# Performance work log

Hardware: AMD Instinct MI355X
Metric: run time of the kernel (lower is better)

Reference implementation:

```python
import jax, jax.numpy as jnp
import numpy as np

EPS = 1e-6

def rms_norm(x, scale):
    # T5-style LayerNorm: RMS over last axis in fp32, then scale
    x32 = x.astype(jnp.float32)
    mean2 = jnp.mean(jnp.square(x32), axis=-1, keepdims=True)
    return (x32 * jax.lax.rsqrt(mean2 + EPS)) * scale

def setup_inputs() -> dict:
    key = jax.random.key(0)
    ks = jax.random.split(key, 7)
    B, S, E, H, D = 2, 2048, 2048, 16, 128
    w_std = 1.0 / np.sqrt(E)
    x = jax.random.normal(ks[0], (B, S, E), jnp.float32)
    wq = jax.random.normal(ks[1], (E, H, D), jnp.float32) * w_std
    wk = jax.random.normal(ks[2], (E, H, D), jnp.float32) * w_std
    wv = jax.random.normal(ks[3], (E, H, D), jnp.float32) * w_std
    wo = jax.random.normal(ks[4], (H, D, E), jnp.float32) * (1.0 / np.sqrt(H * D))
    q_scale = jnp.ones((D,), jnp.float32)
    k_scale = jnp.ones((D,), jnp.float32)
    return {"x": x, "wq": wq, "wk": wk, "wv": wv, "wo": wo,
            "q_scale": q_scale, "k_scale": k_scale}

def reference(x, wq, wk, wv, wo, q_scale, k_scale):
    # Q/K/V projections: [B,S,E] x [E,H,D] -> [B,S,H,D]
    q = jnp.einsum('bse,ehd->bshd', x, wq)
    k = jnp.einsum('bse,ehd->bshd', x, wk)
    v = jnp.einsum('bse,ehd->bshd', x, wv)
    # QK layernorm (RMS, no scaling by 1/sqrt(d) in this variant)
    qn = rms_norm(q, q_scale)
    kn = rms_norm(k, k_scale)
    # Naive attention: explicit [B,H,Q,K] scores
    scores = jnp.einsum('bqhd,bkhd->bhqk', qn, kn)
    attn = jax.nn.softmax(scores, axis=-1)
    out = jnp.einsum('bhqk,bkhd->bqhd', attn, v)
    # Output projection: [B,S,H,D] x [H,D,E] -> [B,S,E]
    return jnp.einsum('bqhd,hde->bqe', out, wo)
```

## Files before the change

### kernel.cpp

```cpp
#include <hip/hip_runtime.h>
#include <hip/hip_bf16.h>
#include <math.h>

#define BATCH 2
#define SEQ   2048
#define EMB   2048
#define NH    16
#define HD    128

typedef __attribute__((ext_vector_type(8))) short short8;
typedef __attribute__((ext_vector_type(8))) _Float16 half8;
typedef __attribute__((ext_vector_type(4))) float floatx4;

__device__ inline void async_load16(const void* g, void* l) {
    __builtin_amdgcn_global_load_lds(
        (const __attribute__((address_space(1))) unsigned int*)g,
        (__attribute__((address_space(3))) unsigned int*)l, 16, 0, 0);
}

__device__ inline unsigned short bf16_bits(float f) {
    __hip_bfloat16 b = __float2bfloat16(f);
    return *(unsigned short*)&b;
}
__device__ inline unsigned short fp16_bits(float f) {
    _Float16 h = (_Float16)f;
    return *(unsigned short*)&h;
}

#define GT 128
#define GK 32

__global__ __launch_bounds__(256) void gemm_bf16(
    const unsigned short* __restrict__ A,
    const unsigned short* __restrict__ Bt,
    float* __restrict__ C, int M, int N, int K)
{
    __shared__ unsigned short As[GT * GK];
    __shared__ unsigned short Bs[GT * GK];

    const int tid  = threadIdx.x;
    const int w    = tid >> 6;
    const int lane = tid & 63;
    const int wr   = w >> 1, wc = w & 1;
    const int row0 = blockIdx.y * GT;
    const int col0 = blockIdx.x * GT;

    floatx4 acc[4][4];
    #pragma unroll
    for (int i = 0; i < 4; i++)
        #pragma unroll
        for (int j = 0; j < 4; j++)
            acc[i][j] = (floatx4){0.f, 0.f, 0.f, 0.f};

    const int srow  = lane >> 2;
    const int skoff = (lane & 3) * 8;
    const int fm = lane & 15;
    const int fk = (lane >> 4) * 8;

    for (int k0 = 0; k0 < K; k0 += GK) {
        #pragma unroll
        for (int t = 0; t < 2; t++) {
            const int c = w * 2 + t;
            async_load16(A  + (size_t)(row0 + c * 16 + srow) * K + k0 + skoff, (char*)As + c * 1024);
            async_load16(Bt + (size_t)(col0 + c * 16 + srow) * K + k0 + skoff, (char*)Bs + c * 1024);
        }
        __syncthreads();

        short8 af[4], bf[4];
        #pragma unroll
        for (int i = 0; i < 4; i++) {
            af[i] = *(const short8*)&As[(wr * 64 + i * 16 + fm) * GK + fk];
            bf[i] = *(const short8*)&Bs[(wc * 64 + i * 16 + fm) * GK + fk];
        }
        #pragma unroll
        for (int i = 0; i < 4; i++)
            #pragma unroll
            for (int j = 0; j < 4; j++)
                acc[i][j] = __builtin_amdgcn_mfma_f32_16x16x32_bf16(af[i], bf[j], acc[i][j], 0, 0, 0);
        __syncthreads();
    }

    const int quad = lane >> 4;
    #pragma unroll
    for (int i = 0; i < 4; i++)
        #pragma unroll
        for (int j = 0; j < 4; j++) {
            const size_t base = (size_t)(row0 + wr * 64 + i * 16 + quad * 4) * N
                              + col0 + wc * 64 + j * 16 + fm;
            #pragma unroll
            for (int r = 0; r < 4; r++)
                C[base + (size_t)r * N] = acc[i][j][r];
        }
}

__global__ __launch_bounds__(256) void gemm_qkv(
    const unsigned short* __restrict__ A,
    const unsigned short* __restrict__ Bq, const unsigned short* __restrict__ Bk,
    const unsigned short* __restrict__ Bv,
    const float* __restrict__ q_scale, const float* __restrict__ k_scale,
    unsigned short* __restrict__ Qf, unsigned short* __restrict__ Kf,
    unsigned short* __restrict__ Vt, int K)
{
    __shared__ char smem[2 * 128 * 72 * 2] __attribute__((aligned(16)));
    unsigned short* As = (unsigned short*)smem;
    unsigned short* Bs = (unsigned short*)(smem + 8192);
    float* ws2f = (float*)(smem + 16384);
    typedef unsigned short stage_row[72];
    stage_row* stage0 = (stage_row*)smem;

    const int z = blockIdx.z;
    const unsigned short* __restrict__ Bt = (z == 0) ? Bq : (z == 1) ? Bk : Bv;

    const int tid  = threadIdx.x;
    const int w    = tid >> 6;
    const int lane = tid & 63;
    const int wr   = w >> 1, wc = w & 1;
    const int row0 = blockIdx.y * GT;
    const int col0 = blockIdx.x * GT;

    floatx4 acc[4][4];
    #pragma unroll
    for (int i = 0; i < 4; i++)
        #pragma unroll
        for (int j = 0; j < 4; j++)
            acc[i][j] = (floatx4){0.f, 0.f, 0.f, 0.f};

    const int srow  = lane >> 2;
    const int skoff = (lane & 3) * 8;
    const int fm = lane & 15;
    const int fk = (lane >> 4) * 8;

    for (int k0 = 0; k0 < K; k0 += GK) {
        #pragma unroll
        for (int t = 0; t < 2; t++) {
            const int c = w * 2 + t;
            async_load16(A  + (size_t)(row0 + c * 16 + srow) * K + k0 + skoff, (char*)As + c * 1024);
            async_load16(Bt + (size_t)(col0 + c * 16 + srow) * K + k0 + skoff, (char*)Bs + c * 1024);
        }
        __syncthreads();

        half8 af[4], bf[4];
        #pragma unroll
        for (int i = 0; i < 4; i++) {
            af[i] = *(const half8*)&As[(wr * 64 + i * 16 + fm) * GK + fk];
            bf[i] = *(const half8*)&Bs[(wc * 64 + i * 16 + fm) * GK + fk];
        }
        #pragma unroll
        for (int i = 0; i < 4; i++)
            #pragma unroll
            for (int j = 0; j < 4; j++)
                acc[i][j] = __builtin_amdgcn_mfma_f32_16x16x32_f16(af[i], bf[j], acc[i][j], 0, 0, 0);
        __syncthreads();
    }

    const int quad = lane >> 4;
    const int hh = col0 >> 7;

    if (z < 2) {
        const float* __restrict__ scale = z ? k_scale : q_scale;
        unsigned short* __restrict__ o = z ? Kf : Qf;

        float sq[4][4];
        #pragma unroll
        for (int i = 0; i < 4; i++)
            #pragma unroll
            for (int r = 0; r < 4; r++) {
                float s2 = 0.f;
                #pragma unroll
                for (int j = 0; j < 4; j++) s2 += acc[i][j][r] * acc[i][j][r];
                s2 += __shfl_xor(s2, 1);
                s2 += __shfl_xor(s2, 2);
                s2 += __shfl_xor(s2, 4);
                s2 += __shfl_xor(s2, 8);
                sq[i][r] = s2;
            }
        if (fm == 0) {
            #pragma unroll
            for (int i = 0; i < 4; i++)
                #pragma unroll
                for (int r = 0; r < 4; r++)
                    ws2f[wc * 128 + wr * 64 + i * 16 + quad * 4 + r] = sq[i][r];
        }
        __syncthreads();

        float scv[4];
        #pragma unroll
        for (int j = 0; j < 4; j++) scv[j] = scale[wc * 64 + j * 16 + fm];

        #pragma unroll
        for (int i = 0; i < 4; i++)
            #pragma unroll
            for (int r = 0; r < 4; r++) {
                const int lrow = wr * 64 + i * 16 + quad * 4 + r;
                const int row  = row0 + lrow;
                const int bb = row >> 11, s = row & 2047;
                const float inv = rsqrtf((ws2f[lrow] + ws2f[128 + lrow]) * (1.0f / HD) + 1e-6f);
                const size_t ob = ((size_t)(bb * NH + hh) * SEQ + s) * 128;
                #pragma unroll
                for (int j = 0; j < 4; j++) {
                    const int d = wc * 64 + j * 16 + fm;
                    const float val = acc[i][j][r] * inv * scv[j];
                    const int dd = z ? ((((d >> 3) ^ (s & 15)) << 3) | (d & 7)) : d;
                    o[ob + dd] = fp16_bits(val);
                }
            }
    } else {
        const int b  = row0 >> 11;
        const int bh = b * NH + hh;
        const int kt_base = (row0 & 2047) >> 6;

        #pragma unroll
        for (int i = 0; i < 4; i++)
            #pragma unroll
            for (int r = 0; r < 4; r++) {
                const int key = i * 16 + quad * 4 + r;
                #pragma unroll
                for (int j = 0; j < 4; j++) {
                    const int d = wc * 64 + j * 16 + fm;
                    stage0[wr * 128 + d][key] = fp16_bits(acc[i][j][r]);
                }
            }
        __syncthreads();

        const int d = tid >> 1, half = tid & 1;
        #pragma unroll
        for (int kt = 0; kt < 2; kt++) {
            const size_t ob = ((size_t)(bh * 32 + kt_base + kt)) * 8192 + (size_t)d * 64;
            #pragma unroll
            for (int cc = 0; cc < 4; cc++) {
                const int cs = half * 4 + cc;
                const int kb = (cs ^ (d & 7)) << 3;
                *(short8*)&Vt[ob + cs * 8] = *(const short8*)&stage0[kt * 128 + d][kb];
            }
        }
    }
}

__global__ __launch_bounds__(256) void prep_all(
    const float* __restrict__ wq, const float* __restrict__ wk,
    const float* __restrict__ wv, const float* __restrict__ wo,
    const float* __restrict__ x,
    unsigned short* __restrict__ wqF, unsigned short* __restrict__ wkF,
    unsigned short* __restrict__ wvF, unsigned short* __restrict__ woT,
    unsigned short* __restrict__ xf)
{
    __shared__ float tile[32][33];
    const int z = blockIdx.z;
    const int tx = threadIdx.x, ty = threadIdx.y;

    if (z == 4) {
        const int blk = blockIdx.y * 64 + blockIdx.x;
        const size_t base = (size_t)blk * 2048 + (ty * 32 + tx) * 8;
        float4 a = *(const float4*)&x[base];
        float4 b = *(const float4*)&x[base + 4];
        ushort4 ha, hb;
        ha.x = fp16_bits(a.x); ha.y = fp16_bits(a.y); ha.z = fp16_bits(a.z); ha.w = fp16_bits(a.w);
        hb.x = fp16_bits(b.x); hb.y = fp16_bits(b.y); hb.z = fp16_bits(b.z); hb.w = fp16_bits(b.w);
        *(ushort4*)&xf[base] = ha;
        *(ushort4*)&xf[base + 4] = hb;
        return;
    }

    const float* __restrict__ W = (z == 0) ? wq : (z == 1) ? wk : (z == 2) ? wv : wo;
    const int k0 = blockIdx.y * 32, n0 = blockIdx.x * 32;
    #pragma unroll
    for (int i = 0; i < 4; i++)
        tile[ty + i * 8][tx] = W[(size_t)(k0 + ty + i * 8) * 2048 + n0 + tx];
    __syncthreads();
    if (z < 3) {
        unsigned short* __restrict__ t = (z == 0) ? wqF : (z == 1) ? wkF : wvF;
        #pragma unroll
        for (int i = 0; i < 4; i++)
            t[(size_t)(n0 + ty + i * 8) * 2048 + k0 + tx] = fp16_bits(tile[tx][ty + i * 8]);
    } else {
        #pragma unroll
        for (int i = 0; i < 4; i++)
            woT[(size_t)(n0 + ty + i * 8) * 2048 + k0 + tx] = bf16_bits(tile[tx][ty + i * 8]);
    }
}

#define ATQ 256
#define ATK 64

__global__ __launch_bounds__(512, 1) void attn14(
    const unsigned short* __restrict__ Qf, const unsigned short* __restrict__ Kf,
    const unsigned short* __restrict__ Vt, __hip_bfloat16* __restrict__ AO)
{
    __shared__ unsigned short Ks[2][ATK * 128];
    __shared__ unsigned short Vts[2][HD * 64];
    __shared__ unsigned short Ps[ATQ * 64];

    const int tid  = threadIdx.x;
    const int w    = tid >> 6;
    const int lane = tid & 63;
    const int quad = lane >> 4;
    const int fm   = lane & 15;
    const int bh = blockIdx.y;
    const int b = bh >> 4, h = bh & 15;
    const int q0 = blockIdx.x * ATQ;

    const size_t hbase = (size_t)(b * NH + h) * SEQ;

    half8 qf[2][4];
    #pragma unroll
    for (int i = 0; i < 2; i++) {
        const size_t row = hbase + q0 + w * 32 + i * 16 + fm;
        #pragma unroll
        for (int kc = 0; kc < 4; kc++)
            qf[i][kc] = *(const half8*)&Qf[row * 128 + kc * 32 + quad * 8];
    }

    floatx4 oacc[2][8];
    #pragma unroll
    for (int i = 0; i < 2; i++)
        #pragma unroll
        for (int df = 0; df < 8; df++)
            oacc[i][df] = (floatx4){0.f, 0.f, 0.f, 0.f};
    float m_[2][4], l_[2][4];
    #pragma unroll
    for (int i = 0; i < 2; i++)
        #pragma unroll
        for (int r = 0; r < 4; r++) { m_[i][r] = -1e30f; l_[i][r] = 0.f; }

    const unsigned short* gk0  = Kf + hbase * 128;
    const unsigned short* gvt0 = Vt + (size_t)bh * 32 * 8192;

    const int ch0 = w * 4;

    #pragma unroll
    for (int c = 0; c < 4; c++) {
        const int ch = ch0 + c;
        const size_t go = (size_t)(ch & 15) * 512 + lane * 8;
        if (ch < 16) async_load16(gk0  + go, (char*)Ks[0]  + ch * 1024);
        else         async_load16(gvt0 + go, (char*)Vts[0] + (ch - 16) * 1024);
    }
    __syncthreads();

    for (int ktile = 0; ktile < SEQ / ATK; ktile++) {
        const int cur = ktile & 1;

        if (ktile + 1 < SEQ / ATK) {
            const unsigned short* gk  = gk0  + (size_t)(ktile + 1) * ATK * 128;
            const unsigned short* gvt = gvt0 + (size_t)(ktile + 1) * 8192;
            #pragma unroll
            for (int c = 0; c < 4; c++) {
                const int ch = ch0 + c;
                const size_t go = (size_t)(ch & 15) * 512 + lane * 8;
                if (ch < 16) async_load16(gk  + go, (char*)Ks[1 - cur]  + ch * 1024);
                else         async_load16(gvt + go, (char*)Vts[1 - cur] + (ch - 16) * 1024);
            }
        }

        floatx4 sacc[2][4];
        #pragma unroll
        for (int i = 0; i < 2; i++)
            #pragma unroll
            for (int jf = 0; jf < 4; jf++)
                sacc[i][jf] = (floatx4){0.f, 0.f, 0.f, 0.f};
        #pragma unroll
        for (int kc = 0; kc < 4; kc++)
            #pragma unroll
            for (int jf = 0; jf < 4; jf++) {
                const int koff = (jf * 16 + fm) * 128 + (((kc * 4 + quad) ^ fm) << 3);
                half8 k8 = *(const half8*)&Ks[cur][koff];
                #pragma unroll
                for (int i = 0; i < 2; i++)
                    sacc[i][jf] = __builtin_amdgcn_mfma_f32_16x16x32_f16(qf[i][kc], k8, sacc[i][jf], 0, 0, 0);
            }

        float alpha_[2][4];
        #pragma unroll
        for (int i = 0; i < 2; i++)
            #pragma unroll
            for (int r = 0; r < 4; r++) {
                float mx = fmaxf(fmaxf(sacc[i][0][r], sacc[i][1][r]),
                                 fmaxf(sacc[i][2][r], sacc[i][3][r]));
                mx = fmaxf(mx, __shfl_xor(mx, 1));
                mx = fmaxf(mx, __shfl_xor(mx, 2));
                mx = fmaxf(mx, __shfl_xor(mx, 4));
                mx = fmaxf(mx, __shfl_xor(mx, 8));
                const float mold = m_[i][r];
                const float mnew = fmaxf(mold, mx);
                const float al = __expf(mold - mnew);
                m_[i][r] = mnew;
                alpha_[i][r] = al;
                float rs = 0.f;
                #pragma unroll
                for (int jf = 0; jf < 4; jf++) {
                    float p = __expf(sacc[i][jf][r] - mnew);
                    sacc[i][jf][r] = p;
                    rs += p;
                }
                rs += __shfl_xor(rs, 1);
                rs += __shfl_xor(rs, 2);
                rs += __shfl_xor(rs, 4);
                rs += __shfl_xor(rs, 8);
                l_[i][r] = l_[i][r] * al + rs;
            }
        #pragma unroll
        for (int i = 0; i < 2; i++)
            #pragma unroll
            for (int df = 0; df < 8; df++)
                #pragma unroll
                for (int r = 0; r < 4; r++)
                    oacc[i][df][r] *= alpha_[i][r];

        #pragma unroll
        for (int i = 0; i < 2; i++)
            #pragma unroll
            for (int jf = 0; jf < 4; jf++)
                #pragma unroll
                for (int r = 0; r < 4; r++) {
                    const int row = w * 32 + i * 16 + quad * 4 + r;
                    const int chunk = jf * 2 + (fm >> 3);
                    const int colp = ((chunk ^ (row & 7)) << 3) | (fm & 7);
                    Ps[row * 64 + colp] = fp16_bits(sacc[i][jf][r]);
                }

        #pragma unroll
        for (int kc2 = 0; kc2 < 2; kc2++) {
            half8 ap[2];
            #pragma unroll
            for (int i = 0; i < 2; i++) {
                const int row = w * 32 + i * 16 + fm;
                ap[i] = *(const half8*)&Ps[row * 64 + (((kc2 * 4 + quad) ^ (row & 7)) << 3)];
            }
            #pragma unroll
            for (int df = 0; df < 8; df++) {
                const int d = df * 16 + fm;
                half8 bv = *(const half8*)&Vts[cur][d * 64 + (((kc2 * 4 + quad) ^ (d & 7)) << 3)];
                #pragma unroll
                for (int i = 0; i < 2; i++)
                    oacc[i][df] = __builtin_amdgcn_mfma_f32_16x16x32_f16(ap[i], bv, oacc[i][df], 0, 0, 0);
            }
        }

        __syncthreads();
    }

    const size_t obase = ((size_t)b * SEQ * NH + h) * HD;
    const size_t rstr = (size_t)NH * HD;
    float linv[2][4];
    #pragma unroll
    for (int i = 0; i < 2; i++)
        #pragma unroll
        for (int r = 0; r < 4; r++) linv[i][r] = 1.0f / l_[i][r];
    #pragma unroll
    for (int i = 0; i < 2; i++)
        #pragma unroll
        for (int df = 0; df < 8; df++)
            #pragma unroll
            for (int r = 0; r < 4; r++) {
                const int row = q0 + w * 32 + i * 16 + quad * 4 + r;
                const int d = df * 16 + fm;
                AO[obase + (size_t)row * rstr + d] = __float2bfloat16(oacc[i][df][r] * linv[i][r]);
            }
}

extern "C" void kernel_launch(void* const* d_in, const int* in_sizes, int n_in,
                              void* d_out, int out_size, void* d_ws, size_t ws_size,
                              hipStream_t stream) {
    const float* x  = (const float*)d_in[0];
    const float* wq = (const float*)d_in[1];
    const float* wk = (const float*)d_in[2];
    const float* wv = (const float*)d_in[3];
    const float* wo = (const float*)d_in[4];
    const float* q_scale = (const float*)d_in[5];
    const float* k_scale = (const float*)d_in[6];
    float* out = (float*)d_out;

    const size_t T = (size_t)BATCH * SEQ * NH * HD;
    const size_t W = (size_t)EMB * NH * HD;

    unsigned short* xf   = (unsigned short*)d_ws;
    unsigned short* aob  = xf + T;
    unsigned short* Qf   = aob + T;
    unsigned short* Kf   = Qf + T;
    unsigned short* Vtb  = Kf + T;
    unsigned short* wqF  = Vtb + T;
    unsigned short* wkF  = wqF + W;
    unsigned short* wvF  = wkF + W;
    unsigned short* woT  = wvF + W;

    const int M = BATCH * SEQ;
    const int N = NH * HD;
    const int K = EMB;

    prep_all<<<dim3(64, 64, 5), dim3(32, 8), 0, stream>>>(
        wq, wk, wv, wo, x, wqF, wkF, wvF, woT, xf);

    gemm_qkv<<<dim3(N / GT, M / GT, 3), 256, 0, stream>>>(
        xf, wqF, wkF, wvF, q_scale, k_scale, Qf, Kf, Vtb, K);

    attn14<<<dim3(SEQ / ATQ, BATCH * NH), 512, 0, stream>>>(Qf, Kf, Vtb, (__hip_bfloat16*)aob);

    gemm_bf16<<<dim3(EMB / GT, M / GT), 256, 0, stream>>>(aob, woT, out, M, EMB, NH * HD);
}
```

Baseline: 494.4 us.

## Fuse Q/K/V GEMMs into one 12-wave block sharing the A tile, add XCD-aware block mapping

The QKV projection now runs as one launch with 768-thread blocks. Each block loads a single A tile and three B tiles, and the three 4-wave groups compute Q, K and V from the shared A tile, so the input activations are read once instead of three times. Blocks are renumbered so neighbouring tiles land on the same XCD for L2 locality, and the attention kernel gets a similar XCD-aware head/query mapping. The cost is a larger LDS footprint, 768-thread blocks that may lower occupancy, and only 8 of 12 waves issuing loads.

```diff
diff --git a/kernel.cpp b/kernel.cpp
--- a/kernel.cpp
+++ b/kernel.cpp
@@ -93,7 +93,7 @@
         }
 }
 
-__global__ __launch_bounds__(256) void gemm_qkv(
+__global__ __launch_bounds__(768) void gemm_qkv_fused(
     const unsigned short* __restrict__ A,
     const unsigned short* __restrict__ Bq, const unsigned short* __restrict__ Bk,
     const unsigned short* __restrict__ Bv,
@@ -101,22 +101,29 @@
     unsigned short* __restrict__ Qf, unsigned short* __restrict__ Kf,
     unsigned short* __restrict__ Vt, int K)
 {
-    __shared__ char smem[2 * 128 * 72 * 2] __attribute__((aligned(16)));
-    unsigned short* As = (unsigned short*)smem;
-    unsigned short* Bs = (unsigned short*)(smem + 8192);
-    float* ws2f = (float*)(smem + 16384);
+    __shared__ char smem[38912] __attribute__((aligned(16)));
+    unsigned short* As  = (unsigned short*)smem;
+    unsigned short* BsQ = (unsigned short*)(smem + 8192);
+    unsigned short* BsK = (unsigned short*)(smem + 16384);
+    unsigned short* BsV = (unsigned short*)(smem + 24576);
+    float* ws2 = (float*)(smem + 36864);
     typedef unsigned short stage_row[72];
     stage_row* stage0 = (stage_row*)smem;
-
-    const int z = blockIdx.z;
-    const unsigned short* __restrict__ Bt = (z == 0) ? Bq : (z == 1) ? Bk : Bv;
 
     const int tid  = threadIdx.x;
     const int w    = tid >> 6;
     const int lane = tid & 63;
-    const int wr   = w >> 1, wc = w & 1;
-    const int row0 = blockIdx.y * GT;
-    const int col0 = blockIdx.x * GT;
+    const int role = w >> 2;
+    const int wq   = w & 3;
+    const int wr   = wq >> 1, wc = wq & 1;
+
+    const int L   = blockIdx.x;
+    const int xcd = L & 7;
+    const int idx = L >> 3;
+    const int bx  = (xcd & 1) * 8 + (idx & 7);
+    const int by  = (xcd >> 1) * 8 + (idx >> 3);
+    const int row0 = by * GT;
+    const int col0 = bx * GT;
 
     floatx4 acc[4][4];
     #pragma unroll
@@ -131,14 +138,24 @@
     const int fk = (lane >> 4) * 8;
 
     for (int k0 = 0; k0 < K; k0 += GK) {
-        #pragma unroll
-        for (int t = 0; t < 2; t++) {
-            const int c = w * 2 + t;
-            async_load16(A  + (size_t)(row0 + c * 16 + srow) * K + k0 + skoff, (char*)As + c * 1024);
-            async_load16(Bt + (size_t)(col0 + c * 16 + srow) * K + k0 + skoff, (char*)Bs + c * 1024);
+        if (w < 8) {
+            #pragma unroll
+            for (int c = 0; c < 4; c++) {
+                const int ch  = w * 4 + c;
+                const int sub = ch & 7;
+                const int base = (ch < 8) ? row0 : col0;
+                const size_t off = (size_t)(base + sub * 16 + srow) * K + k0 + skoff;
+                switch (ch >> 3) {
+                    case 0:  async_load16(A  + off, (char*)As  + sub * 1024); break;
+                    case 1:  async_load16(Bq + off, (char*)BsQ + sub * 1024); break;
+                    case 2:  async_load16(Bk + off, (char*)BsK + sub * 1024); break;
+                    default: async_load16(Bv + off, (char*)BsV + sub * 1024); break;
+                }
+            }
         }
         __syncthreads();
 
+        const unsigned short* __restrict__ Bs = (role == 0) ? BsQ : (role == 1) ? BsK : BsV;
         half8 af[4], bf[4];
         #pragma unroll
         for (int i = 0; i < 4; i++) {
@@ -156,10 +173,7 @@
     const int quad = lane >> 4;
     const int hh = col0 >> 7;
 
-    if (z < 2) {
-        const float* __restrict__ scale = z ? k_scale : q_scale;
-        unsigned short* __restrict__ o = z ? Kf : Qf;
-
+    if (role < 2) {
         float sq[4][4];
         #pragma unroll
         for (int i = 0; i < 4; i++)
@@ -179,10 +193,26 @@
             for (int i = 0; i < 4; i++)
                 #pragma unroll
                 for (int r = 0; r < 4; r++)
-                    ws2f[wc * 128 + wr * 64 + i * 16 + quad * 4 + r] = sq[i][r];
-        }
-        __syncthreads();
-
+                    ws2[(role * 2 + wc) * 128 + wr * 64 + i * 16 + quad * 4 + r] = sq[i][r];
+        }
+    } else {
+        #pragma unroll
+        for (int i = 0; i < 4; i++)
+            #pragma unroll
+            for (int r = 0; r < 4; r++) {
+                const int key = i * 16 + quad * 4 + r;
+                #pragma unroll
+                for (int j = 0; j < 4; j++) {
+                    const int d = wc * 64 + j * 16 + fm;
+                    stage0[wr * 128 + d][key] = fp16_bits(acc[i][j][r]);
+                }
+            }
+    }
+    __syncthreads();
+
+    if (role < 2) {
+        const float* __restrict__ scale = role ? k_scale : q_scale;
+        unsigned short* __restrict__ o = role ? Kf : Qf;
         float scv[4];
         #pragma unroll
         for (int j = 0; j < 4; j++) scv[j] = scale[wc * 64 + j * 16 + fm];
@@ -194,13 +224,13 @@
                 const int lrow = wr * 64 + i * 16 + quad * 4 + r;
                 const int row  = row0 + lrow;
                 const int bb = row >> 11, s = row & 2047;
-                const float inv = rsqrtf((ws2f[lrow] + ws2f[128 + lrow]) * (1.0f / HD) + 1e-6f);
+                const float inv = rsqrtf((ws2[role * 2 * 128 + lrow] + ws2[(role * 2 + 1) * 128 + lrow]) * (1.0f / HD) + 1e-6f);
                 const size_t ob = ((size_t)(bb * NH + hh) * SEQ + s) * 128;
                 #pragma unroll
                 for (int j = 0; j < 4; j++) {
                     const int d = wc * 64 + j * 16 + fm;
                     const float val = acc[i][j][r] * inv * scv[j];
-                    const int dd = z ? ((((d >> 3) ^ (s & 15)) << 3) | (d & 7)) : d;
+                    const int dd = role ? ((((d >> 3) ^ (s & 15)) << 3) | (d & 7)) : d;
                     o[ob + dd] = fp16_bits(val);
                 }
             }
@@ -208,27 +238,14 @@
         const int b  = row0 >> 11;
         const int bh = b * NH + hh;
         const int kt_base = (row0 & 2047) >> 6;
-
-        #pragma unroll
-        for (int i = 0; i < 4; i++)
-            #pragma unroll
-            for (int r = 0; r < 4; r++) {
-                const int key = i * 16 + quad * 4 + r;
-                #pragma unroll
-                for (int j = 0; j < 4; j++) {
-                    const int d = wc * 64 + j * 16 + fm;
-                    stage0[wr * 128 + d][key] = fp16_bits(acc[i][j][r]);
-                }
-            }
-        __syncthreads();
-
-        const int d = tid >> 1, half = tid & 1;
+        const int vtid = tid & 255;
+        const int d = vtid >> 1, half_ = vtid & 1;
         #pragma unroll
         for (int kt = 0; kt < 2; kt++) {
             const size_t ob = ((size_t)(bh * 32 + kt_base + kt)) * 8192 + (size_t)d * 64;
             #pragma unroll
             for (int cc = 0; cc < 4; cc++) {
-                const int cs = half * 4 + cc;
+                const int cs = half_ * 4 + cc;
                 const int kb = (cs ^ (d & 7)) << 3;
                 *(short8*)&Vt[ob + cs * 8] = *(const short8*)&stage0[kt * 128 + d][kb];
             }
@@ -295,9 +312,13 @@
     const int lane = tid & 63;
     const int quad = lane >> 4;
     const int fm   = lane & 15;
-    const int bh = blockIdx.y;
+
+    const int L   = blockIdx.x;
+    const int xcd = L & 7;
+    const int g   = L >> 3;
+    const int bh  = xcd * 4 + (g & 3);
+    const int q0  = (g >> 2) * ATQ;
     const int b = bh >> 4, h = bh & 15;
-    const int q0 = blockIdx.x * ATQ;
 
     const size_t hbase = (size_t)(b * NH + h) * SEQ;
 
@@ -489,10 +510,10 @@
     prep_all<<<dim3(64, 64, 5), dim3(32, 8), 0, stream>>>(
         wq, wk, wv, wo, x, wqF, wkF, wvF, woT, xf);
 
-    gemm_qkv<<<dim3(N / GT, M / GT, 3), 256, 0, stream>>>(
+    gemm_qkv_fused<<<512, 768, 0, stream>>>(
         xf, wqF, wkF, wvF, q_scale, k_scale, Qf, Kf, Vtb, K);
 
-    attn14<<<dim3(SEQ / ATQ, BATCH * NH), 512, 0, stream>>>(Qf, Kf, Vtb, (__hip_bfloat16*)aob);
+    attn14<<<256, 512, 0, stream>>>(Qf, Kf, Vtb, (__hip_bfloat16*)aob);
 
     gemm_bf16<<<dim3(EMB / GT, M / GT), 256, 0, stream>>>(aob, woT, out, M, EMB, NH * HD);
 }
```

After: 505.4 us. 2.2% more time.
